# Performance work log

Measured on AMD Instinct MI355X. Metric: run time of the kernel, lower is better.

The kernel has to match this reference:

```python
import jax, jax.numpy as jnp
import numpy as np

E, IN, HID, OUT, B = 8, 512, 512, 512, 1024
BN_EPS = 1e-5

def _init_w(key, e, i, o):
    bound = np.sqrt(6.0 / (i * o))
    return jax.random.uniform(key, (e, i, o), dtype=jnp.float32, minval=-bound, maxval=bound)

def setup_inputs() -> dict:
    key = jax.random.key(0)
    k = jax.random.split(key, 6)
    x = jax.random.normal(k[0], (B, IN), dtype=jnp.float32)
    coef = jax.random.uniform(k[1], (B, E), dtype=jnp.float32)
    coef = coef / jnp.sum(coef, axis=-1, keepdims=True)  # soft blending weights
    w1 = _init_w(k[2], E, IN, HID)
    b1 = jnp.zeros((E, HID), dtype=jnp.float32)
    w2 = _init_w(k[3], E, HID, OUT)
    b2 = jnp.zeros((E, OUT), dtype=jnp.float32)
    gamma = jnp.ones((HID,), dtype=jnp.float32)
    beta = jnp.zeros((HID,), dtype=jnp.float32)
    return {"x": x, "blending_coef": coef, "w1": w1, "b1": b1,
            "w2": w2, "b2": b2, "gamma": gamma, "beta": beta}

def reference(x, blending_coef, w1, b1, w2, b2, gamma, beta):
    # layer 1: per-sample blended linear. Same math as
    # sum(coef[...,None,None]*w1, dim=1) applied via sum(x[...,None]*W, dim=1),
    # expressed as one contraction to avoid the [B,I,H] intermediate.
    h = jnp.einsum('be,eih,bi->bh', blending_coef, w1, x) + blending_coef @ b1
    # BatchNorm1d (training mode: batch stats, biased variance) + affine
    mean = jnp.mean(h, axis=0)
    var = jnp.mean((h - mean) ** 2, axis=0)
    hn = (h - mean) * jax.lax.rsqrt(var + BN_EPS) * gamma + beta
    h1 = jax.nn.elu(hn)
    # layer 2
    out = jnp.einsum('be,eho,bh->bo', blending_coef, w2, h1) + blending_coef @ b2
    return out
```

## Files before the change

kernel.cpp:

```cpp
#include <hip/hip_runtime.h>


typedef short bf16x8 __attribute__((ext_vector_type(8)));
typedef float f32x4 __attribute__((ext_vector_type(4)));
typedef unsigned short u16;
typedef u16 u16x8 __attribute__((ext_vector_type(8)));

__device__ __forceinline__ u16 f2bf(float f) {
  union { float f; unsigned u; } v; v.f = f;
  return (u16)((v.u + 0x7FFFu + ((v.u >> 16) & 1u)) >> 16);
}
__device__ __forceinline__ float bf2f(u16 u) {
  union { unsigned u; float f; } v; v.u = (unsigned)u << 16; return v.f;
}

__global__ __launch_bounds__(256) void prep1_kernel(
    const float* __restrict__ x, const float* __restrict__ w1,
    u16* __restrict__ xbp, u16* __restrict__ w1p)
{
  int bid = blockIdx.x, t = threadIdx.x;
  __shared__ float ld[64][65];
  if (bid < 64) {
    int g = bid, ri = t & 15, q = t >> 4;
    #pragma unroll
    for (int rep = 0; rep < 4; ++rep) {
      int chunk = rep * 16 + q;
      int s = chunk >> 2, c = chunk & 3;
      const float* src = x + (size_t)(g * 16 + ri) * 512 + s * 32 + c * 8;
      f32x4 v0 = *(const f32x4*)src;
      f32x4 v1 = *(const f32x4*)(src + 4);
      u16x8 o;
      #pragma unroll
      for (int i = 0; i < 4; ++i) { o[i] = f2bf(v0[i]); o[4 + i] = f2bf(v1[i]); }
      *(u16x8*)(xbp + ((size_t)(g * 16 + s) * 64 + c * 16 + ri) * 8) = o;
    }
    return;
  }
  int job = bid - 64;
  int e = job >> 6, tl = job & 63;
  int kt = tl >> 3, nt = tl & 7;
  #pragma unroll
  for (int j = 0; j < 4; ++j) {
    int kr = j * 16 + (t >> 4), nc = (t & 15) * 4;
    f32x4 v = *(const f32x4*)(w1 + (size_t)(e * 512 + kt * 64 + kr) * 512 + nt * 64 + nc);
    ld[kr][nc] = v.x; ld[kr][nc + 1] = v.y; ld[kr][nc + 2] = v.z; ld[kr][nc + 3] = v.w;
  }
  __syncthreads();
  #pragma unroll
  for (int rep = 0; rep < 2; ++rep) {
    int gidx = rep * 256 + t;
    int ri = gidx & 15, c = (gidx >> 4) & 3, sl = (gidx >> 6) & 1, grp = gidx >> 7;
    int n_local = grp * 16 + ri;
    int gn = nt * 4 + grp, s = kt * 2 + sl, k0 = sl * 32 + c * 8;
    u16x8 o;
    #pragma unroll
    for (int i = 0; i < 8; ++i) o[i] = f2bf(ld[k0 + i][n_local]);
    *(u16x8*)(w1p + ((size_t)((e * 32 + gn) * 16 + s) * 64 + c * 16 + ri) * 8) = o;
  }
}

__global__ __launch_bounds__(512, 2) void gemm1_prep2(
    const u16* __restrict__ Ap, const u16* __restrict__ Wp,
    const float* __restrict__ coef, const float* __restrict__ bias,
    const float* __restrict__ w2, u16* __restrict__ w2p,
    u16* __restrict__ hb, float* __restrict__ sP, float* __restrict__ qP)
{
  __shared__ __align__(16) char smem[38912];
  int t = threadIdx.x;
  if (blockIdx.x >= 256) {
    float (*ld)[65] = (float (*)[65])smem;
    int job = blockIdx.x - 256;
    int e = job >> 6, tl = job & 63;
    int kt = tl >> 3, nt = tl & 7;
    #pragma unroll
    for (int j = 0; j < 2; ++j) {
      int kr = j * 32 + (t >> 4), nc = (t & 15) * 4;
      f32x4 v = *(const f32x4*)(w2 + (size_t)(e * 512 + kt * 64 + kr) * 512 + nt * 64 + nc);
      ld[kr][nc] = v.x; ld[kr][nc + 1] = v.y; ld[kr][nc + 2] = v.z; ld[kr][nc + 3] = v.w;
    }
    __syncthreads();
    {
      int ri = t & 15, c = (t >> 4) & 3, sl = (t >> 6) & 1, grp = t >> 7;
      int n_local = grp * 16 + ri;
      int gn = nt * 4 + grp, s = kt * 2 + sl, k0 = sl * 32 + c * 8;
      u16x8 o;
      #pragma unroll
      for (int i = 0; i < 8; ++i) o[i] = f2bf(ld[k0 + i][n_local]);
      *(u16x8*)(w2p + ((size_t)((e * 32 + gn) * 16 + s) * 64 + c * 16 + ri) * 8) = o;
    }
    return;
  }
  float* red = (float*)smem;
  int raw = blockIdx.x, nt = raw & 7, mt = raw >> 3;
  int l = t & 63, e = t >> 6;

  const u16* Ab = Ap + (size_t)(mt * 2) * 16 * 512 + l * 8;
  const u16* Bb = Wp + (size_t)(e * 32 + nt * 4) * 16 * 512 + l * 8;

  f32x4 acc[2][4] = {};
  bf16x8 bfr[2][4];
  #pragma unroll
  for (int n = 0; n < 4; ++n)
    bfr[0][n] = *(const bf16x8*)(Bb + (size_t)n * 16 * 512);

  #pragma unroll
  for (int s = 0; s < 16; ++s) {
    const int cur = s & 1, nxt = cur ^ 1;
    if (s < 15) {
      #pragma unroll
      for (int n = 0; n < 4; ++n)
        bfr[nxt][n] = *(const bf16x8*)(Bb + (size_t)n * 16 * 512 + (s + 1) * 512);
    }
    bf16x8 af[2];
    #pragma unroll
    for (int m = 0; m < 2; ++m)
      af[m] = *(const bf16x8*)(Ab + (size_t)m * 16 * 512 + s * 512);
    #pragma unroll
    for (int m = 0; m < 2; ++m)
      #pragma unroll
      for (int n = 0; n < 4; ++n)
        acc[m][n] = __builtin_amdgcn_mfma_f32_16x16x32_bf16(af[m], bfr[cur][n], acc[m][n], 0, 0, 0);
  }

  int rl = (l >> 4) * 4;
  #pragma unroll
  for (int m = 0; m < 2; ++m)
    #pragma unroll
    for (int r = 0; r < 4; ++r) {
      float cf = coef[(size_t)(mt * 32 + m * 16 + rl + r) * 8 + e];
      #pragma unroll
      for (int n = 0; n < 4; ++n) acc[m][n][r] *= cf;
    }

#define RED_STORE(slot)                                                       \
  { _Pragma("unroll") for (int m = 0; m < 2; ++m)                             \
    _Pragma("unroll") for (int n = 0; n < 4; ++n)                             \
    _Pragma("unroll") for (int r = 0; r < 4; ++r)                             \
      red[(slot) * 2176 + (m * 16 + rl + r) * 68 + n * 16 + (l & 15)] = acc[m][n][r]; }
#define RED_ADD(slot)                                                         \
  { _Pragma("unroll") for (int m = 0; m < 2; ++m)                             \
    _Pragma("unroll") for (int n = 0; n < 4; ++n)                             \
    _Pragma("unroll") for (int r = 0; r < 4; ++r)                             \
      acc[m][n][r] += red[(slot) * 2176 + (m * 16 + rl + r) * 68 + n * 16 + (l & 15)]; }

  if (e >= 4) RED_STORE(e - 4);
  __syncthreads();
  if (e < 4) RED_ADD(e);
  __syncthreads();
  if (e == 2 || e == 3) RED_STORE(e - 2);
  __syncthreads();
  if (e < 2) RED_ADD(e);
  __syncthreads();
  if (e == 1) RED_STORE(0);
  __syncthreads();

  if (e == 0) {
    RED_ADD(0);
    int col0 = nt * 64;
    float bcol[4][8];
    #pragma unroll
    for (int n = 0; n < 4; ++n)
      #pragma unroll
      for (int e2 = 0; e2 < 8; ++e2)
        bcol[n][e2] = bias[e2 * 512 + col0 + n * 16 + (l & 15)];
    float sS[4] = {0.f, 0.f, 0.f, 0.f}, sQ[4] = {0.f, 0.f, 0.f, 0.f};
    #pragma unroll
    for (int m = 0; m < 2; ++m)
      #pragma unroll
      for (int r = 0; r < 4; ++r) {
        int rowg = mt * 32 + m * 16 + rl + r;
        f32x4 c0 = *(const f32x4*)(coef + (size_t)rowg * 8);
        f32x4 c1 = *(const f32x4*)(coef + (size_t)rowg * 8 + 4);
        #pragma unroll
        for (int n = 0; n < 4; ++n) {
          float bb = c0[0]*bcol[n][0] + c0[1]*bcol[n][1] + c0[2]*bcol[n][2] + c0[3]*bcol[n][3]
                   + c1[0]*bcol[n][4] + c1[1]*bcol[n][5] + c1[2]*bcol[n][6] + c1[3]*bcol[n][7];
          float v = acc[m][n][r] + bb;
          red[(m * 16 + rl + r) * 68 + n * 16 + (l & 15)] = v;
          if (true) { sS[n] += v; sQ[n] += v * v; }
        }
      }
    #pragma unroll
    for (int n = 0; n < 4; ++n) {
      sS[n] += __shfl_xor(sS[n], 16); sS[n] += __shfl_xor(sS[n], 32);
      sQ[n] += __shfl_xor(sQ[n], 16); sQ[n] += __shfl_xor(sQ[n], 32);
    }
    if (l < 16) {
      #pragma unroll
      for (int n = 0; n < 4; ++n) {
        sP[mt * 512 + col0 + n * 16 + l] = sS[n];
        qP[mt * 512 + col0 + n * 16 + l] = sQ[n];
      }
    }
    asm volatile("s_waitcnt lgkmcnt(0)" ::: "memory");
    __builtin_amdgcn_sched_barrier(0);
    int c = l >> 4, ri = l & 15;
    #pragma unroll
    for (int g = 0; g < 2; ++g)
      #pragma unroll
      for (int sr = 0; sr < 2; ++sr) {
        f32x4 a = *(const f32x4*)&red[(g * 16 + ri) * 68 + sr * 32 + c * 8];
        f32x4 b = *(const f32x4*)&red[(g * 16 + ri) * 68 + sr * 32 + c * 8 + 4];
        u16x8 o;
        #pragma unroll
        for (int i = 0; i < 4; ++i) { o[i] = f2bf(a[i]); o[4 + i] = f2bf(b[i]); }
        *(u16x8*)(hb + ((size_t)((mt * 2 + g) * 16 + nt * 2 + sr) * 64 + c * 16 + ri) * 8) = o;
      }
  }
#undef RED_STORE
#undef RED_ADD
}

__global__ __launch_bounds__(512, 2) void gemm2_kernel(
    const u16* __restrict__ hb, const u16* __restrict__ Wp,
    const float* __restrict__ coef, const float* __restrict__ bias,
    const float* __restrict__ gamma, const float* __restrict__ beta,
    const float* __restrict__ sP, const float* __restrict__ qP,
    float* __restrict__ Out)
{
  __shared__ __align__(16) char smem[38912];
  __shared__ float sc[512], sh[512];
  u16* As = (u16*)smem;
  float* red = (float*)smem;
  int raw = blockIdx.x, nt = raw & 7, mt = raw >> 3;
  int t = threadIdx.x, l = t & 63, e = t >> 6;

  const u16* Bb = Wp + (size_t)(e * 32 + nt * 4) * 16 * 512 + l * 8;
  bf16x8 bfr[2][4];
  #pragma unroll
  for (int n = 0; n < 4; ++n)
    bfr[0][n] = *(const bf16x8*)(Bb + (size_t)n * 16 * 512);

  {
    float S = 0.f, Q = 0.f;
    #pragma unroll
    for (int p = 0; p < 32; ++p) { S += sP[p * 512 + t]; Q += qP[p * 512 + t]; }
    float mean = S * (1.0f / 1024.0f);
    float var  = Q * (1.0f / 1024.0f) - mean * mean;
    float s_ = gamma[t] * rsqrtf(var + 1e-5f);
    sc[t] = s_; sh[t] = beta[t] - mean * s_;
  }
  __syncthreads();

  const u16* hsrc = hb + (size_t)mt * 16384;
  #pragma unroll
  for (int rep = 0; rep < 4; ++rep) {
    int ci = rep * 512 + t;
    u16x8 hv = *(const u16x8*)(hsrc + (size_t)ci * 8);
    int s = (ci >> 6) & 15, c = (l >> 4) & 3;
    int k0 = s * 32 + c * 8;
    f32x4 s0 = *(const f32x4*)&sc[k0], s1 = *(const f32x4*)&sc[k0 + 4];
    f32x4 h0 = *(const f32x4*)&sh[k0], h1 = *(const f32x4*)&sh[k0 + 4];
    u16x8 o;
    #pragma unroll
    for (int i = 0; i < 4; ++i) {
      float v = bf2f(hv[i]) * s0[i] + h0[i];
      o[i] = f2bf(v > 0.f ? v : expm1f(v));
    }
    #pragma unroll
    for (int i = 0; i < 4; ++i) {
      float v = bf2f(hv[4 + i]) * s1[i] + h1[i];
      o[4 + i] = f2bf(v > 0.f ? v : expm1f(v));
    }
    *(u16x8*)&As[(size_t)ci * 8] = o;
  }
  __syncthreads();

  f32x4 acc[2][4] = {};
  #pragma unroll
  for (int s = 0; s < 16; ++s) {
    const int cur = s & 1, nxt = cur ^ 1;
    if (s < 15) {
      #pragma unroll
      for (int n = 0; n < 4; ++n)
        bfr[nxt][n] = *(const bf16x8*)(Bb + (size_t)n * 16 * 512 + (s + 1) * 512);
    }
    bf16x8 af[2];
    #pragma unroll
    for (int m = 0; m < 2; ++m)
      af[m] = *(const bf16x8*)&As[((m * 16 + s) * 64 + l) * 8];
    #pragma unroll
    for (int m = 0; m < 2; ++m)
      #pragma unroll
      for (int n = 0; n < 4; ++n)
        acc[m][n] = __builtin_amdgcn_mfma_f32_16x16x32_bf16(af[m], bfr[cur][n], acc[m][n], 0, 0, 0);
  }
  __syncthreads();

  int rl = (l >> 4) * 4;
  #pragma unroll
  for (int m = 0; m < 2; ++m)
    #pragma unroll
    for (int r = 0; r < 4; ++r) {
      float cf = coef[(size_t)(mt * 32 + m * 16 + rl + r) * 8 + e];
      #pragma unroll
      for (int n = 0; n < 4; ++n) acc[m][n][r] *= cf;
    }

#define RED_STORE(slot)                                                       \
  { _Pragma("unroll") for (int m = 0; m < 2; ++m)                             \
    _Pragma("unroll") for (int n = 0; n < 4; ++n)                             \
    _Pragma("unroll") for (int r = 0; r < 4; ++r)                             \
      red[(slot) * 2176 + (m * 16 + rl + r) * 68 + n * 16 + (l & 15)] = acc[m][n][r]; }
#define RED_ADD(slot)                                                         \
  { _Pragma("unroll") for (int m = 0; m < 2; ++m)                             \
    _Pragma("unroll") for (int n = 0; n < 4; ++n)                             \
    _Pragma("unroll") for (int r = 0; r < 4; ++r)                             \
      acc[m][n][r] += red[(slot) * 2176 + (m * 16 + rl + r) * 68 + n * 16 + (l & 15)]; }

  if (e >= 4) RED_STORE(e - 4);
  __syncthreads();
  if (e < 4) RED_ADD(e);
  __syncthreads();
  if (e == 2 || e == 3) RED_STORE(e - 2);
  __syncthreads();
  if (e < 2) RED_ADD(e);
  __syncthreads();
  if (e == 1) RED_STORE(0);
  __syncthreads();

  if (e == 0) {
    RED_ADD(0);
    int col0 = nt * 64;
    float bcol[4][8];
    #pragma unroll
    for (int n = 0; n < 4; ++n)
      #pragma unroll
      for (int e2 = 0; e2 < 8; ++e2)
        bcol[n][e2] = bias[e2 * 512 + col0 + n * 16 + (l & 15)];
    #pragma unroll
    for (int m = 0; m < 2; ++m)
      #pragma unroll
      for (int r = 0; r < 4; ++r) {
        int rowg = mt * 32 + m * 16 + rl + r;
        f32x4 c0 = *(const f32x4*)(coef + (size_t)rowg * 8);
        f32x4 c1 = *(const f32x4*)(coef + (size_t)rowg * 8 + 4);
        #pragma unroll
        for (int n = 0; n < 4; ++n) {
          float bb = c0[0]*bcol[n][0] + c0[1]*bcol[n][1] + c0[2]*bcol[n][2] + c0[3]*bcol[n][3]
                   + c1[0]*bcol[n][4] + c1[1]*bcol[n][5] + c1[2]*bcol[n][6] + c1[3]*bcol[n][7];
          Out[(size_t)rowg * 512 + col0 + n * 16 + (l & 15)] = acc[m][n][r] + bb;
        }
      }
  }
#undef RED_STORE
#undef RED_ADD
}

extern "C" void kernel_launch(void* const* d_in, const int* in_sizes, int n_in,
                              void* d_out, int out_size, void* d_ws, size_t ws_size,
                              hipStream_t stream)
{
  const float* x     = (const float*)d_in[0];
  const float* coef  = (const float*)d_in[1];
  const float* w1    = (const float*)d_in[2];
  const float* b1    = (const float*)d_in[3];
  const float* w2    = (const float*)d_in[4];
  const float* b2    = (const float*)d_in[5];
  const float* gamma = (const float*)d_in[6];
  const float* beta  = (const float*)d_in[7];
  float* out = (float*)d_out;

  char* ws = (char*)d_ws;
  u16* w1p  = (u16*)(ws);
  u16* w2p  = (u16*)(ws + (4u << 20));
  u16* xbp  = (u16*)(ws + (8u << 20));
  u16* hb   = (u16*)(ws + (9u << 20));
  float* sP = (float*)(ws + (10u << 20));
  float* qP = (float*)(ws + (10u << 20) + 65536);

  prep1_kernel<<<576, 256, 0, stream>>>(x, w1, xbp, w1p);
  gemm1_prep2<<<768, 512, 0, stream>>>(xbp, w1p, coef, b1, w2, w2p, hb, sP, qP);
  gemm2_kernel<<<256, 512, 0, stream>>>(hb, w2p, coef, b2, gamma, beta, sP, qP, out);
}
```

Baseline: 39.99 us.

## Flatten cross-wave expert reduction and deepen operand prefetch in both GEMMs

```diff
diff --git a/kernel.cpp b/kernel.cpp
--- a/kernel.cpp
+++ b/kernel.cpp
@@ -4,6 +4,7 @@
 typedef short bf16x8 __attribute__((ext_vector_type(8)));
 typedef float f32x4 __attribute__((ext_vector_type(4)));
 typedef unsigned short u16;
+typedef u16 u16x4 __attribute__((ext_vector_type(4)));
 typedef u16 u16x8 __attribute__((ext_vector_type(8)));
 
 __device__ __forceinline__ u16 f2bf(float f) {
@@ -91,6 +92,8 @@
     return;
   }
   float* red = (float*)smem;
+  f32x4* partS = (f32x4*)(smem + 34816);
+  f32x4* partQ = (f32x4*)(smem + 34816 + 2048);
   int raw = blockIdx.x, nt = raw & 7, mt = raw >> 3;
   int l = t & 63, e = t >> 6;
 
@@ -98,28 +101,34 @@
   const u16* Bb = Wp + (size_t)(e * 32 + nt * 4) * 16 * 512 + l * 8;
 
   f32x4 acc[2][4] = {};
-  bf16x8 bfr[2][4];
-  #pragma unroll
-  for (int n = 0; n < 4; ++n)
+  bf16x8 bfr[3][4], afr[2][2];
+  #pragma unroll
+  for (int n = 0; n < 4; ++n) {
     bfr[0][n] = *(const bf16x8*)(Bb + (size_t)n * 16 * 512);
+    bfr[1][n] = *(const bf16x8*)(Bb + (size_t)n * 16 * 512 + 512);
+  }
+  #pragma unroll
+  for (int m = 0; m < 2; ++m)
+    afr[0][m] = *(const bf16x8*)(Ab + (size_t)m * 16 * 512);
 
   #pragma unroll
   for (int s = 0; s < 16; ++s) {
-    const int cur = s & 1, nxt = cur ^ 1;
+    const int cb = s % 3, nb = (s + 2) % 3, ca = s & 1, na = ca ^ 1;
+    if (s < 14) {
+      #pragma unroll
+      for (int n = 0; n < 4; ++n)
+        bfr[nb][n] = *(const bf16x8*)(Bb + (size_t)n * 16 * 512 + (s + 2) * 512);
+    }
     if (s < 15) {
       #pragma unroll
+      for (int m = 0; m < 2; ++m)
+        afr[na][m] = *(const bf16x8*)(Ab + (size_t)m * 16 * 512 + (s + 1) * 512);
+    }
+    #pragma unroll
+    for (int m = 0; m < 2; ++m)
+      #pragma unroll
       for (int n = 0; n < 4; ++n)
-        bfr[nxt][n] = *(const bf16x8*)(Bb + (size_t)n * 16 * 512 + (s + 1) * 512);
-    }
-    bf16x8 af[2];
-    #pragma unroll
-    for (int m = 0; m < 2; ++m)
-      af[m] = *(const bf16x8*)(Ab + (size_t)m * 16 * 512 + s * 512);
-    #pragma unroll
-    for (int m = 0; m < 2; ++m)
-      #pragma unroll
-      for (int n = 0; n < 4; ++n)
-        acc[m][n] = __builtin_amdgcn_mfma_f32_16x16x32_bf16(af[m], bfr[cur][n], acc[m][n], 0, 0, 0);
+        acc[m][n] = __builtin_amdgcn_mfma_f32_16x16x32_bf16(afr[ca][m], bfr[cb][n], acc[m][n], 0, 0, 0);
   }
 
   int rl = (l >> 4) * 4;
@@ -145,67 +154,45 @@
 
   if (e >= 4) RED_STORE(e - 4);
   __syncthreads();
-  if (e < 4) RED_ADD(e);
-  __syncthreads();
-  if (e == 2 || e == 3) RED_STORE(e - 2);
-  __syncthreads();
-  if (e < 2) RED_ADD(e);
-  __syncthreads();
-  if (e == 1) RED_STORE(0);
-  __syncthreads();
-
-  if (e == 0) {
-    RED_ADD(0);
-    int col0 = nt * 64;
-    float bcol[4][8];
-    #pragma unroll
-    for (int n = 0; n < 4; ++n)
-      #pragma unroll
-      for (int e2 = 0; e2 < 8; ++e2)
-        bcol[n][e2] = bias[e2 * 512 + col0 + n * 16 + (l & 15)];
-    float sS[4] = {0.f, 0.f, 0.f, 0.f}, sQ[4] = {0.f, 0.f, 0.f, 0.f};
-    #pragma unroll
-    for (int m = 0; m < 2; ++m)
-      #pragma unroll
-      for (int r = 0; r < 4; ++r) {
-        int rowg = mt * 32 + m * 16 + rl + r;
-        f32x4 c0 = *(const f32x4*)(coef + (size_t)rowg * 8);
-        f32x4 c1 = *(const f32x4*)(coef + (size_t)rowg * 8 + 4);
-        #pragma unroll
-        for (int n = 0; n < 4; ++n) {
-          float bb = c0[0]*bcol[n][0] + c0[1]*bcol[n][1] + c0[2]*bcol[n][2] + c0[3]*bcol[n][3]
-                   + c1[0]*bcol[n][4] + c1[1]*bcol[n][5] + c1[2]*bcol[n][6] + c1[3]*bcol[n][7];
-          float v = acc[m][n][r] + bb;
-          red[(m * 16 + rl + r) * 68 + n * 16 + (l & 15)] = v;
-          if (true) { sS[n] += v; sQ[n] += v * v; }
-        }
-      }
-    #pragma unroll
-    for (int n = 0; n < 4; ++n) {
-      sS[n] += __shfl_xor(sS[n], 16); sS[n] += __shfl_xor(sS[n], 32);
-      sQ[n] += __shfl_xor(sQ[n], 16); sQ[n] += __shfl_xor(sQ[n], 32);
-    }
-    if (l < 16) {
-      #pragma unroll
-      for (int n = 0; n < 4; ++n) {
-        sP[mt * 512 + col0 + n * 16 + l] = sS[n];
-        qP[mt * 512 + col0 + n * 16 + l] = sQ[n];
-      }
-    }
-    asm volatile("s_waitcnt lgkmcnt(0)" ::: "memory");
-    __builtin_amdgcn_sched_barrier(0);
-    int c = l >> 4, ri = l & 15;
-    #pragma unroll
-    for (int g = 0; g < 2; ++g)
-      #pragma unroll
-      for (int sr = 0; sr < 2; ++sr) {
-        f32x4 a = *(const f32x4*)&red[(g * 16 + ri) * 68 + sr * 32 + c * 8];
-        f32x4 b = *(const f32x4*)&red[(g * 16 + ri) * 68 + sr * 32 + c * 8 + 4];
-        u16x8 o;
-        #pragma unroll
-        for (int i = 0; i < 4; ++i) { o[i] = f2bf(a[i]); o[4 + i] = f2bf(b[i]); }
-        *(u16x8*)(hb + ((size_t)((mt * 2 + g) * 16 + nt * 2 + sr) * 64 + c * 16 + ri) * 8) = o;
-      }
+  if (e < 4) { RED_ADD(e); RED_STORE(e); }
+  __syncthreads();
+
+  {
+    int row = t >> 4, c0 = (t & 15) * 4;
+    f32x4 v = {0.f, 0.f, 0.f, 0.f};
+    #pragma unroll
+    for (int sl = 0; sl < 4; ++sl)
+      v += *(const f32x4*)&red[sl * 2176 + row * 68 + c0];
+    int rowg = mt * 32 + row, colg = nt * 64 + c0;
+    f32x4 cv0 = *(const f32x4*)(coef + (size_t)rowg * 8);
+    f32x4 cv1 = *(const f32x4*)(coef + (size_t)rowg * 8 + 4);
+    #pragma unroll
+    for (int e2 = 0; e2 < 4; ++e2) {
+      v += cv0[e2] * *(const f32x4*)(bias + e2 * 512 + colg);
+      v += cv1[e2] * *(const f32x4*)(bias + (e2 + 4) * 512 + colg);
+    }
+    f32x4 ss = v, qq = v * v;
+    #pragma unroll
+    for (int i = 0; i < 4; ++i) {
+      ss[i] += __shfl_xor(ss[i], 16); ss[i] += __shfl_xor(ss[i], 32);
+      qq[i] += __shfl_xor(qq[i], 16); qq[i] += __shfl_xor(qq[i], 32);
+    }
+    int w = t >> 6;
+    if (l < 16) { partS[w * 16 + l] = ss; partQ[w * 16 + l] = qq; }
+    u16x4 o;
+    #pragma unroll
+    for (int i = 0; i < 4; ++i) o[i] = f2bf(v[i]);
+    int g = row >> 4, ri = row & 15;
+    int spk = nt * 2 + (c0 >> 5), cpk = (c0 >> 3) & 3, j = c0 & 7;
+    *(u16x4*)(hb + ((size_t)((mt * 2 + g) * 16 + spk) * 64 + cpk * 16 + ri) * 8 + j) = o;
+  }
+  __syncthreads();
+  if (t < 16) {
+    f32x4 S = {0.f, 0.f, 0.f, 0.f}, Q = {0.f, 0.f, 0.f, 0.f};
+    #pragma unroll
+    for (int w = 0; w < 8; ++w) { S += partS[w * 16 + t]; Q += partQ[w * 16 + t]; }
+    *(f32x4*)(sP + mt * 512 + nt * 64 + t * 4) = S;
+    *(f32x4*)(qP + mt * 512 + nt * 64 + t * 4) = Q;
   }
 #undef RED_STORE
 #undef RED_ADD
@@ -218,7 +205,7 @@
     const float* __restrict__ sP, const float* __restrict__ qP,
     float* __restrict__ Out)
 {
-  __shared__ __align__(16) char smem[38912];
+  __shared__ __align__(16) char smem[34816];
   __shared__ float sc[512], sh[512];
   u16* As = (u16*)smem;
   float* red = (float*)smem;
@@ -226,10 +213,12 @@
   int t = threadIdx.x, l = t & 63, e = t >> 6;
 
   const u16* Bb = Wp + (size_t)(e * 32 + nt * 4) * 16 * 512 + l * 8;
-  bf16x8 bfr[2][4];
-  #pragma unroll
-  for (int n = 0; n < 4; ++n)
+  bf16x8 bfr[3][4];
+  #pragma unroll
+  for (int n = 0; n < 4; ++n) {
     bfr[0][n] = *(const bf16x8*)(Bb + (size_t)n * 16 * 512);
+    bfr[1][n] = *(const bf16x8*)(Bb + (size_t)n * 16 * 512 + 512);
+  }
 
   {
     float S = 0.f, Q = 0.f;
@@ -269,11 +258,11 @@
   f32x4 acc[2][4] = {};
   #pragma unroll
   for (int s = 0; s < 16; ++s) {
-    const int cur = s & 1, nxt = cur ^ 1;
-    if (s < 15) {
+    const int cb = s % 3, nb = (s + 2) % 3;
+    if (s < 14) {
       #pragma unroll
       for (int n = 0; n < 4; ++n)
-        bfr[nxt][n] = *(const bf16x8*)(Bb + (size_t)n * 16 * 512 + (s + 1) * 512);
+        bfr[nb][n] = *(const bf16x8*)(Bb + (size_t)n * 16 * 512 + (s + 2) * 512);
     }
     bf16x8 af[2];
     #pragma unroll
@@ -283,7 +272,7 @@
     for (int m = 0; m < 2; ++m)
       #pragma unroll
       for (int n = 0; n < 4; ++n)
-        acc[m][n] = __builtin_amdgcn_mfma_f32_16x16x32_bf16(af[m], bfr[cur][n], acc[m][n], 0, 0, 0);
+        acc[m][n] = __builtin_amdgcn_mfma_f32_16x16x32_bf16(af[m], bfr[cb][n], acc[m][n], 0, 0, 0);
   }
   __syncthreads();
 
@@ -310,38 +299,24 @@
 
   if (e >= 4) RED_STORE(e - 4);
   __syncthreads();
-  if (e < 4) RED_ADD(e);
-  __syncthreads();
-  if (e == 2 || e == 3) RED_STORE(e - 2);
-  __syncthreads();
-  if (e < 2) RED_ADD(e);
-  __syncthreads();
-  if (e == 1) RED_STORE(0);
-  __syncthreads();
-
-  if (e == 0) {
-    RED_ADD(0);
-    int col0 = nt * 64;
-    float bcol[4][8];
-    #pragma unroll
-    for (int n = 0; n < 4; ++n)
-      #pragma unroll
-      for (int e2 = 0; e2 < 8; ++e2)
-        bcol[n][e2] = bias[e2 * 512 + col0 + n * 16 + (l & 15)];
-    #pragma unroll
-    for (int m = 0; m < 2; ++m)
-      #pragma unroll
-      for (int r = 0; r < 4; ++r) {
-        int rowg = mt * 32 + m * 16 + rl + r;
-        f32x4 c0 = *(const f32x4*)(coef + (size_t)rowg * 8);
-        f32x4 c1 = *(const f32x4*)(coef + (size_t)rowg * 8 + 4);
-        #pragma unroll
-        for (int n = 0; n < 4; ++n) {
-          float bb = c0[0]*bcol[n][0] + c0[1]*bcol[n][1] + c0[2]*bcol[n][2] + c0[3]*bcol[n][3]
-                   + c1[0]*bcol[n][4] + c1[1]*bcol[n][5] + c1[2]*bcol[n][6] + c1[3]*bcol[n][7];
-          Out[(size_t)rowg * 512 + col0 + n * 16 + (l & 15)] = acc[m][n][r] + bb;
-        }
-      }
+  if (e < 4) { RED_ADD(e); RED_STORE(e); }
+  __syncthreads();
+
+  {
+    int row = t >> 4, c0 = (t & 15) * 4;
+    f32x4 v = {0.f, 0.f, 0.f, 0.f};
+    #pragma unroll
+    for (int sl = 0; sl < 4; ++sl)
+      v += *(const f32x4*)&red[sl * 2176 + row * 68 + c0];
+    int rowg = mt * 32 + row, colg = nt * 64 + c0;
+    f32x4 cv0 = *(const f32x4*)(coef + (size_t)rowg * 8);
+    f32x4 cv1 = *(const f32x4*)(coef + (size_t)rowg * 8 + 4);
+    #pragma unroll
+    for (int e2 = 0; e2 < 4; ++e2) {
+      v += cv0[e2] * *(const f32x4*)(bias + e2 * 512 + colg);
+      v += cv1[e2] * *(const f32x4*)(bias + (e2 + 4) * 512 + colg);
+    }
+    *(f32x4*)(Out + (size_t)rowg * 512 + colg) = v;
   }
 #undef RED_STORE
 #undef RED_ADD
```

Measured after the change: 40.10 us. Within noise of the previous version (+0.3%).
